# Kernel tuning notes

Measured on AMD Instinct MI355X. Metric: run time of the kernel, lower is better.

The kernel has to match this reference:

```python
import jax, jax.numpy as jnp
import numpy as np

# dims (match init_kwargs / input_specs)
D = 768      # embed_dim
H = 12       # num query heads
G = 4        # num kv groups
E = 8        # num experts
K = 2        # experts per token
F = 4 * D    # ffn hidden dim
B, S, T = 2, 1024, 1024
DH = D // H  # head dim = 64
EPS = 1e-6


def setup_inputs() -> dict:
    key = jax.random.key(0)
    ks = jax.random.split(key, 16)

    def p(k, shape, scale=0.02):
        return jax.random.normal(k, shape, jnp.float32) * scale

    inp = {}
    inp['x'] = jax.random.normal(ks[0], (B, S, D), jnp.float32)
    inp['encoder_context'] = jax.random.normal(ks[1], (B, T, D), jnp.float32)
    for n in ('ln1', 'ln2', 'ln3'):
        inp[n + '_scale'] = jnp.ones((D,), jnp.float32)
        inp[n + '_bias'] = jnp.zeros((D,), jnp.float32)
    i = 2
    for pre in ('sa', 'ca'):
        inp[pre + '_wq'] = p(ks[i], (D, H * DH)); i += 1
        inp[pre + '_bq'] = jnp.zeros((H * DH,), jnp.float32)
        inp[pre + '_wk'] = p(ks[i], (D, G * DH)); i += 1
        inp[pre + '_bk'] = jnp.zeros((G * DH,), jnp.float32)
        inp[pre + '_wv'] = p(ks[i], (D, G * DH)); i += 1
        inp[pre + '_bv'] = jnp.zeros((G * DH,), jnp.float32)
        inp[pre + '_wo'] = p(ks[i], (H * DH, D)); i += 1
        inp[pre + '_bo'] = jnp.zeros((D,), jnp.float32)
    inp['gate_w'] = p(ks[i], (D, E)); i += 1
    inp['gate_b'] = jnp.zeros((E,), jnp.float32)
    inp['w1'] = p(ks[i], (E, D, F)); i += 1
    inp['b1'] = jnp.zeros((E, F), jnp.float32)
    inp['w2'] = p(ks[i], (E, F, D)); i += 1
    inp['b2'] = jnp.zeros((E, D), jnp.float32)
    return inp


def _ln(x, scale, bias):
    mu = jnp.mean(x, axis=-1, keepdims=True)
    var = jnp.mean(jnp.square(x - mu), axis=-1, keepdims=True)
    return (x - mu) * jax.lax.rsqrt(var + EPS) * scale + bias


def _gqa(q_in, kv_in, wq, bq, wk, bk, wv, bv, wo, bo, causal):
    Bq, Sq, _ = q_in.shape
    Skv = kv_in.shape[1]
    q = (q_in @ wq + bq).reshape(Bq, Sq, H, DH)
    k = (kv_in @ wk + bk).reshape(Bq, Skv, G, DH)
    v = (kv_in @ wv + bv).reshape(Bq, Skv, G, DH)
    rep = H // G
    k = jnp.repeat(k, rep, axis=2)  # [B,Skv,H,DH]
    v = jnp.repeat(v, rep, axis=2)
    scores = jnp.einsum('bqhd,bkhd->bhqk', q, k) / jnp.sqrt(jnp.asarray(DH, q.dtype))
    if causal:
        cmask = jnp.tril(jnp.ones((Sq, Skv), bool))
        scores = jnp.where(cmask[None, None], scores, jnp.finfo(scores.dtype).min)
    attn = jax.nn.softmax(scores, axis=-1)
    out = jnp.einsum('bhqk,bkhd->bqhd', attn, v).reshape(Bq, Sq, H * DH)
    return out @ wo + bo


def _moe(x, gate_w, gate_b, w1, b1, w2, b2):
    logits = x @ gate_w + gate_b                      # [B,S,E]
    probs = jax.nn.softmax(logits, axis=-1)
    top_v, top_i = jax.lax.top_k(probs, K)            # [B,S,K]
    top_v = top_v / jnp.sum(top_v, axis=-1, keepdims=True)
    combine = jnp.sum(jax.nn.one_hot(top_i, E, dtype=x.dtype) * top_v[..., None], axis=-2)  # [B,S,E]
    h = jax.nn.gelu(jnp.einsum('bsd,edf->ebsf', x, w1) + b1[:, None, None, :])
    y = jnp.einsum('ebsf,efd->ebsd', h, w2) + b2[:, None, None, :]
    return jnp.einsum('ebsd,bse->bsd', y, combine)


def reference(x, encoder_context,
              ln1_scale, ln1_bias, ln2_scale, ln2_bias, ln3_scale, ln3_bias,
              sa_wq, sa_bq, sa_wk, sa_bk, sa_wv, sa_bv, sa_wo, sa_bo,
              ca_wq, ca_bq, ca_wk, ca_bk, ca_wv, ca_bv, ca_wo, ca_bo,
              gate_w, gate_b, w1, b1, w2, b2):
    xn = _ln(x, ln1_scale, ln1_bias)
    x = x + _gqa(xn, xn, sa_wq, sa_bq, sa_wk, sa_bk, sa_wv, sa_bv, sa_wo, sa_bo, causal=True)
    xn = _ln(x, ln2_scale, ln2_bias)
    x = x + _gqa(xn, encoder_context, ca_wq, ca_bq, ca_wk, ca_bk, ca_wv, ca_bv, ca_wo, ca_bo, causal=False)
    xn = _ln(x, ln3_scale, ln3_bias)
    x = x + _moe(xn, gate_w, gate_b, w1, b1, w2, b2)
    return x
```

## Files before the change

### kernel.cpp

```cpp
#include <hip/hip_runtime.h>

#define DEV __device__ __forceinline__

typedef __attribute__((ext_vector_type(4))) float f32x4;
typedef __attribute__((ext_vector_type(8))) short short8;
typedef __attribute__((ext_vector_type(4))) unsigned int u32x4;
typedef __attribute__((ext_vector_type(4))) unsigned short us16x4;

#define D_ 768
#define S_ 1024
#define B_ 2
#define H_ 12
#define G_ 4
#define DH_ 64
#define E_ 8
#define F_ 3072
#define NTOK (B_*S_)

#define GLDS16(g, l) __builtin_amdgcn_global_load_lds( \
    (const __attribute__((address_space(1))) void*)(g), \
    (__attribute__((address_space(3))) void*)(l), 16, 0, 0)

DEV unsigned short f2bf(float f){
  unsigned int b = __float_as_uint(f);
  b += 0x7FFFu + ((b >> 16) & 1u);
  return (unsigned short)(b >> 16);
}
DEV float bf2f(unsigned short h){ return __uint_as_float(((unsigned int)h) << 16); }
DEV unsigned int splitbf_pack(float v){
  unsigned short h = f2bf(v);
  unsigned short l = f2bf(v - bf2f(h));
  return (unsigned int)h | ((unsigned int)l << 16);
}

DEV short8 lds_swz(const unsigned short* base, int row, int chunk){
  return *(const short8*)((const char*)base + row*128 + (((chunk ^ (row & 7)) << 4)));
}

DEV void swz_decode(int Fb, int nPanels, int& m, int& panel){
  int xcd = Fb & 7;
  int a = Fb >> 3;
  int mi = a & 3;
  int pid = (a >> 2)*8 + xcd;
  m = (pid / nPanels)*4 + mi;
  panel = pid % nPanels;
}

__global__ __launch_bounds__(256) void tcast_kernel(const float* __restrict__ W,
                                                    unsigned short* __restrict__ Wh,
                                                    unsigned short* __restrict__ Wl,
                                                    int K, int N){
  __shared__ float tile[32][33];
  long long zoff = (long long)blockIdx.z * K * N;
  const float* Wz = W + zoff;
  int n0 = blockIdx.x*32, k0 = blockIdx.y*32;
  int tx = threadIdx.x, ty = threadIdx.y;
  #pragma unroll
  for (int i=0;i<4;i++){
    int r = ty + i*8;
    tile[r][tx] = Wz[(long long)(k0+r)*N + n0 + tx];
  }
  __syncthreads();
  #pragma unroll
  for (int i=0;i<4;i++){
    int r = ty + i*8;
    float v = tile[tx][r];
    unsigned int hl = splitbf_pack(v);
    long long o = zoff + (long long)(n0+r)*K + k0 + tx;
    Wh[o] = (unsigned short)(hl & 0xFFFFu);
    if (Wl) Wl[o] = (unsigned short)(hl >> 16);
  }
}

__global__ void split_rows(const float* __restrict__ in, int ld, int width,
                           unsigned short* __restrict__ hi, unsigned short* __restrict__ lo){
  long long t = blockIdx.x;
  int c = threadIdx.x*4;
  f32x4 v = *(const f32x4*)(in + t*ld + c);
  unsigned int p0 = splitbf_pack(v.x), p1 = splitbf_pack(v.y);
  unsigned int p2 = splitbf_pack(v.z), p3 = splitbf_pack(v.w);
  us16x4 h, l;
  h.x=(unsigned short)p0; l.x=(unsigned short)(p0>>16);
  h.y=(unsigned short)p1; l.y=(unsigned short)(p1>>16);
  h.z=(unsigned short)p2; l.z=(unsigned short)(p2>>16);
  h.w=(unsigned short)p3; l.w=(unsigned short)(p3>>16);
  *(us16x4*)(hi + t*width + c) = h;
  *(us16x4*)(lo + t*width + c) = l;
}

__global__ void concat_bias(const float* __restrict__ b0, int n0,
                            const float* __restrict__ b1, int n1,
                            const float* __restrict__ b2, int n2,
                            float* __restrict__ out){
  int i = blockIdx.x*256 + threadIdx.x;
  if (i < n0) out[i] = b0[i];
  else if (i < n0+n1) out[i] = b1[i-n0];
  else if (i < n0+n1+n2) out[i] = b2[i-n0-n1];
}

__global__ __launch_bounds__(256) void ln_kernel(const float* __restrict__ x,
                                                 const float* __restrict__ sc,
                                                 const float* __restrict__ bi,
                                                 unsigned short* __restrict__ outh,
                                                 unsigned short* __restrict__ outl,
                                                 float* __restrict__ outf){
  __shared__ float red[8];
  long long row = blockIdx.x;
  const float* xr = x + row*D_;
  int tid = threadIdx.x;
  float v0 = xr[tid], v1 = xr[tid+256], v2 = xr[tid+512];
  float s = v0+v1+v2;
  float q = v0*v0 + v1*v1 + v2*v2;
  #pragma unroll
  for (int off=32; off; off>>=1){ s += __shfl_xor(s, off); q += __shfl_xor(q, off); }
  int lane = tid & 63, w = tid >> 6;
  if (lane == 0){ red[w] = s; red[4+w] = q; }
  __syncthreads();
  s = red[0]+red[1]+red[2]+red[3];
  q = red[4]+red[5]+red[6]+red[7];
  float mu  = s * (1.0f/D_);
  float var = q * (1.0f/D_) - mu*mu;
  float rstd = rsqrtf(var + 1e-6f);
  #pragma unroll
  for (int i=0;i<3;i++){
    int idx = tid + 256*i;
    float vv = (i==0) ? v0 : (i==1) ? v1 : v2;
    float o = (vv - mu)*rstd*sc[idx] + bi[idx];
    unsigned int pk = splitbf_pack(o);
    outh[row*D_ + idx] = (unsigned short)(pk & 0xFFFFu);
    if (outl) outl[row*D_ + idx] = (unsigned short)(pk >> 16);
    if (outf) outf[row*D_ + idx] = o;
  }
}

__global__ __launch_bounds__(256) void gemm3(
    int nX,
    const unsigned short* __restrict__ Ah, const unsigned short* __restrict__ Al, int lda,
    const unsigned short* __restrict__ Wh, const unsigned short* __restrict__ Wl, int K,
    const float* __restrict__ bias,
    const float* __restrict__ resid, int ldr,
    float* __restrict__ Cf, int ldc)
{
  __shared__ __align__(16) unsigned short AshH[128*64];
  __shared__ __align__(16) unsigned short AshL[128*64];
  __shared__ __align__(16) unsigned short BshH[64*64];
  __shared__ __align__(16) unsigned short BshL[64*64];
  int mB, panel;
  swz_decode(blockIdx.x, nX, mB, panel);
  const int r0 = mB*128;
  const int n0 = panel*64;
  const int tid = threadIdx.x;
  const int lane = tid & 63;
  const int wv = tid >> 6;
  const int wr = (wv>>1)*64, wc = (wv&1)*32;
  const int l15 = lane & 15, l4 = lane >> 4;
  const int sr = lane >> 3;
  const int sc = (lane & 7) ^ sr;

  f32x4 acc[4][2];
  #pragma unroll
  for (int i=0;i<4;i++)
    #pragma unroll
    for (int j=0;j<2;j++) acc[i][j] = (f32x4){0.f,0.f,0.f,0.f};

  for (int k0 = 0; k0 < K; k0 += 64){
    #pragma unroll
    for (int i=0;i<4;i++){
      int seg = wv*4 + i;
      long long src = (long long)(r0 + seg*8 + sr)*lda + k0 + sc*8;
      GLDS16(Ah + src, AshH + seg*8*64);
      GLDS16(Al + src, AshL + seg*8*64);
    }
    #pragma unroll
    for (int i=0;i<2;i++){
      int seg = wv*2 + i;
      long long src = (long long)(n0 + seg*8 + sr)*K + k0 + sc*8;
      GLDS16(Wh + src, BshH + seg*8*64);
      GLDS16(Wl + src, BshL + seg*8*64);
    }
    __syncthreads();
    #pragma unroll
    for (int ks=0; ks<2; ks++){
      int chunk = ks*4 + l4;
      short8 bh[2], bl[2];
      #pragma unroll
      for (int fj=0; fj<2; fj++){
        bh[fj] = lds_swz(BshH, wc + fj*16 + l15, chunk);
        bl[fj] = lds_swz(BshL, wc + fj*16 + l15, chunk);
      }
      #pragma unroll
      for (int fi=0; fi<4; fi++){
        short8 ah = lds_swz(AshH, wr + fi*16 + l15, chunk);
        short8 al = lds_swz(AshL, wr + fi*16 + l15, chunk);
        #pragma unroll
        for (int fj=0; fj<2; fj++){
          acc[fi][fj] = __builtin_amdgcn_mfma_f32_16x16x32_bf16(ah, bh[fj], acc[fi][fj], 0,0,0);
          acc[fi][fj] = __builtin_amdgcn_mfma_f32_16x16x32_bf16(al, bh[fj], acc[fi][fj], 0,0,0);
          acc[fi][fj] = __builtin_amdgcn_mfma_f32_16x16x32_bf16(ah, bl[fj], acc[fi][fj], 0,0,0);
        }
      }
    }
    __syncthreads();
  }

  #pragma unroll
  for (int fi=0; fi<4; fi++)
  #pragma unroll
  for (int fj=0; fj<2; fj++)
  #pragma unroll
  for (int reg=0; reg<4; reg++){
    int r = r0 + wr + fi*16 + l4*4 + reg;
    int col = n0 + wc + fj*16 + l15;
    float val = acc[fi][fj][reg] + bias[col];
    if (resid) val += resid[(long long)r*ldr + col];
    Cf[(long long)r*ldc + col] = val;
  }
}

__global__ __launch_bounds__(256) void gemm_nt128(
    int nX, int nzPerE,
    const unsigned short* __restrict__ A, int lda,
    const unsigned short* __restrict__ Wt, long long wstride,
    const float* __restrict__ bias, int bias_stride,
    const int* __restrict__ counts,
    const int* __restrict__ a_idx, int a_idx_stride,
    const int* __restrict__ row_base,
    float* __restrict__ Cf, long long partStride,
    unsigned short* __restrict__ Cb, int ldc,
    int K, int do_gelu)
{
  __shared__ __align__(16) unsigned short As[128*64];
  __shared__ __align__(16) unsigned short Bs[128*64];
  int mB, panel;
  swz_decode(blockIdx.x, nX*E_*nzPerE, mB, panel);
  const int n0 = (panel % nX)*128;
  const int zI = panel / nX;
  const int z = zI / nzPerE;
  const int kp = zI % nzPerE;
  const int Mz = counts[z];
  const int r0 = mB*128;
  if (r0 >= Mz) return;
  const int obase = row_base[z];
  const unsigned short* Wz = Wt + (long long)z*wstride;
  const float* bz = bias + (long long)z*bias_stride;
  const int kLen = K / nzPerE;
  const int kBeg = kp * kLen;
  const int tid = threadIdx.x;
  const int lane = tid & 63;
  const int wv = tid >> 6;
  const int wr = (wv>>1)*64, wc = (wv&1)*64;
  const int l15 = lane & 15, l4 = lane >> 4;
  const int sr = lane >> 3;
  const int sc = (lane & 7) ^ sr;

  long long arow[4];
  #pragma unroll
  for (int i=0;i<4;i++){
    int seg = wv*4 + i;
    int r = r0 + seg*8 + sr;
    int rcl = (r < Mz) ? r : (Mz-1);
    arow[i] = a_idx ? (long long)a_idx[(long long)z*a_idx_stride + rcl]
                    : (long long)(obase + rcl);
  }

  f32x4 acc[4][4];
  #pragma unroll
  for (int i=0;i<4;i++)
    #pragma unroll
    for (int j=0;j<4;j++) acc[i][j] = (f32x4){0.f,0.f,0.f,0.f};

  for (int k0 = kBeg; k0 < kBeg + kLen; k0 += 64){
    #pragma unroll
    for (int i=0;i<4;i++){
      int seg = wv*4 + i;
      GLDS16(A + arow[i]*lda + k0 + sc*8, As + seg*8*64);
      GLDS16(Wz + (long long)(n0 + seg*8 + sr)*K + k0 + sc*8, Bs + seg*8*64);
    }
    __syncthreads();
    #pragma unroll
    for (int ks=0; ks<2; ks++){
      int chunk = ks*4 + l4;
      short8 a[4], b[4];
      #pragma unroll
      for (int f=0; f<4; f++){
        a[f] = lds_swz(As, wr + f*16 + l15, chunk);
        b[f] = lds_swz(Bs, wc + f*16 + l15, chunk);
      }
      #pragma unroll
      for (int fi=0; fi<4; fi++)
        #pragma unroll
        for (int fj=0; fj<4; fj++)
          acc[fi][fj] = __builtin_amdgcn_mfma_f32_16x16x32_bf16(a[fi], b[fj], acc[fi][fj], 0,0,0);
    }
    __syncthreads();
  }

  #pragma unroll
  for (int fi=0; fi<4; fi++)
  #pragma unroll
  for (int fj=0; fj<4; fj++)
  #pragma unroll
  for (int reg=0; reg<4; reg++){
    int r = r0 + wr + fi*16 + l4*4 + reg;
    if (r >= Mz) continue;
    int col = n0 + wc + fj*16 + l15;
    float val = acc[fi][fj][reg] + (kp == 0 ? bz[col] : 0.0f);
    if (do_gelu){
      float xx = val;
      float u = 0.7978845608028654f*(xx + 0.044715f*xx*xx*xx);
      float t = 1.0f - 2.0f/(__expf(2.0f*u) + 1.0f);
      val = 0.5f*xx*(1.0f + t);
    }
    long long orow = (long long)obase + r;
    if (Cf) Cf[kp*partStride + orow*ldc + col] = val;
    if (Cb) Cb[orow*ldc + col] = f2bf(val);
  }
}

__global__ __launch_bounds__(256) void vt_split_kernel(const float* __restrict__ vin,
                                                       int ld, int cofs,
                                                       unsigned short* __restrict__ vth,
                                                       unsigned short* __restrict__ vtl){
  __shared__ float tile[32][33];
  int s0 = blockIdx.x*32, d0 = blockIdx.y*32;
  int bg = blockIdx.z; int b = bg >> 2, g = bg & 3;
  int tx = threadIdx.x, ty = threadIdx.y;
  #pragma unroll
  for (int i=0;i<4;i++){
    int r = ty + i*8;
    tile[r][tx] = vin[(long long)(b*1024 + s0 + r)*ld + cofs + g*64 + d0 + tx];
  }
  __syncthreads();
  #pragma unroll
  for (int i=0;i<4;i++){
    int d = d0 + ty + i*8;
    unsigned int pk = splitbf_pack(tile[tx][ty + i*8]);
    long long o = (long long)(bg*64 + d)*1024 + s0 + tx;
    vth[o] = (unsigned short)(pk & 0xFFFFu);
    vtl[o] = (unsigned short)(pk >> 16);
  }
}

#define AT_LDK 72
#define AT_LDP 76
__global__ __launch_bounds__(256, 2) void attn_mfma(
    const float* __restrict__ q, int qld,
    const unsigned short* __restrict__ kh, const unsigned short* __restrict__ kl,
    const unsigned short* __restrict__ vth, const unsigned short* __restrict__ vtl,
    unsigned short* __restrict__ ctxh, unsigned short* __restrict__ ctxl, int causal)
{
  __shared__ __align__(16) unsigned short KhS[64*AT_LDK];
  __shared__ __align__(16) unsigned short KlS[64*AT_LDK];
  __shared__ __align__(16) unsigned short VhS[64*AT_LDK];
  __shared__ __align__(16) unsigned short VlS[64*AT_LDK];
  __shared__ __align__(16) unsigned int   Pp[4][16*AT_LDP];

  const int qblk = blockIdx.x;
  const int h = blockIdx.y;
  const int b = blockIdx.z;
  const int g = h / (H_/G_);
  const int tid = threadIdx.x;
  const int lane = tid & 63;
  const int w = tid >> 6;
  const int l15 = lane & 15;
  const int l4 = lane >> 4;
  const int qb0 = qblk*64;

  short8 qh[2], ql[2];
  #pragma unroll
  for (int ks=0; ks<2; ks++){
    const float* qp = q + ((long long)(b*S_ + qb0 + w*16 + l15))*qld + h*DH_ + ks*32 + l4*8;
    f32x4 q0 = *(const f32x4*)qp;
    f32x4 q1 = *(const f32x4*)(qp + 4);
    float qq[8] = {q0.x,q0.y,q0.z,q0.w,q1.x,q1.y,q1.z,q1.w};
    #pragma unroll
    for (int j=0;j<8;j++){
      unsigned int pk = splitbf_pack(qq[j]*0.125f);
      qh[ks][j] = (short)(pk & 0xFFFFu);
      ql[ks][j] = (short)(pk >> 16);
    }
  }

  f32x4 o[4];
  #pragma unroll
  for (int fd=0; fd<4; fd++) o[fd] = (f32x4){0.f,0.f,0.f,0.f};
  float m[4]    = {-3.0e38f,-3.0e38f,-3.0e38f,-3.0e38f};
  float lsum[4] = {0.f,0.f,0.f,0.f};

  const int ntiles = causal ? (qblk + 1) : (S_/64);
  for (int kt=0; kt<ntiles; kt++){
    __syncthreads();
    {
      int r = tid >> 2, c = tid & 3;
      long long krow = (long long)(b*S_ + kt*64 + r)*(G_*DH_) + g*DH_;
      long long vrow = (long long)((b*G_ + g)*64 + r)*S_ + kt*64;
      *(u32x4*)&KhS[r*AT_LDK + c*8]     = *(const u32x4*)(kh + krow + c*8);
      *(u32x4*)&KhS[r*AT_LDK + (c+4)*8] = *(const u32x4*)(kh + krow + (c+4)*8);
      *(u32x4*)&KlS[r*AT_LDK + c*8]     = *(const u32x4*)(kl + krow + c*8);
      *(u32x4*)&KlS[r*AT_LDK + (c+4)*8] = *(const u32x4*)(kl + krow + (c+4)*8);
      *(u32x4*)&VhS[r*AT_LDK + c*8]     = *(const u32x4*)(vth + vrow + c*8);
      *(u32x4*)&VhS[r*AT_LDK + (c+4)*8] = *(const u32x4*)(vth + vrow + (c+4)*8);
      *(u32x4*)&VlS[r*AT_LDK + c*8]     = *(const u32x4*)(vtl + vrow + c*8);
      *(u32x4*)&VlS[r*AT_LDK + (c+4)*8] = *(const u32x4*)(vtl + vrow + (c+4)*8);
    }
    __syncthreads();

    f32x4 s[4];
    #pragma unroll
    for (int fj=0; fj<4; fj++) s[fj] = (f32x4){0.f,0.f,0.f,0.f};
    #pragma unroll
    for (int ks=0; ks<2; ks++){
      #pragma unroll
      for (int fj=0; fj<4; fj++){
        short8 bh = *(const short8*)&KhS[(fj*16 + l15)*AT_LDK + ks*32 + l4*8];
        short8 bl = *(const short8*)&KlS[(fj*16 + l15)*AT_LDK + ks*32 + l4*8];
        s[fj] = __builtin_amdgcn_mfma_f32_16x16x32_bf16(qh[ks], bh, s[fj], 0,0,0);
        s[fj] = __builtin_amdgcn_mfma_f32_16x16x32_bf16(ql[ks], bh, s[fj], 0,0,0);
        s[fj] = __builtin_amdgcn_mfma_f32_16x16x32_bf16(qh[ks], bl, s[fj], 0,0,0);
      }
    }

    if (causal && kt == qblk){
      #pragma unroll
      for (int fj=0; fj<4; fj++){
        int key = kt*64 + fj*16 + l15;
        #pragma unroll
        for (int reg=0; reg<4; reg++){
          int qr = qb0 + w*16 + l4*4 + reg;
          if (key > qr) s[fj][reg] = -3.0e38f;
        }
      }
    }

    float c[4], pmax[4];
    #pragma unroll
    for (int reg=0; reg<4; reg++){
      float mx = fmaxf(fmaxf(s[0][reg], s[1][reg]), fmaxf(s[2][reg], s[3][reg]));
      mx = fmaxf(mx, __shfl_xor(mx, 1));
      mx = fmaxf(mx, __shfl_xor(mx, 2));
      mx = fmaxf(mx, __shfl_xor(mx, 4));
      mx = fmaxf(mx, __shfl_xor(mx, 8));
      float mn = fmaxf(m[reg], mx);
      c[reg] = __expf(m[reg] - mn);
      m[reg] = mn;
      pmax[reg] = mn;
    }
    float psum[4] = {0.f,0.f,0.f,0.f};
    #pragma unroll
    for (int fj=0; fj<4; fj++){
      #pragma unroll
      for (int reg=0; reg<4; reg++){
        float pv = __expf(s[fj][reg] - pmax[reg]);
        psum[reg] += pv;
        Pp[w][(l4*4 + reg)*AT_LDP + fj*16 + l15] = splitbf_pack(pv);
      }
    }
    #pragma unroll
    for (int reg=0; reg<4; reg++){
      float ps = psum[reg];
      ps += __shfl_xor(ps, 1); ps += __shfl_xor(ps, 2);
      ps += __shfl_xor(ps, 4); ps += __shfl_xor(ps, 8);
      lsum[reg] = lsum[reg]*c[reg] + ps;
      o[0][reg] *= c[reg]; o[1][reg] *= c[reg];
      o[2][reg] *= c[reg]; o[3][reg] *= c[reg];
    }

    #pragma unroll
    for (int ks=0; ks<2; ks++){
      u32x4 pa = *(const u32x4*)&Pp[w][l15*AT_LDP + ks*32 + l4*8];
      u32x4 pb = *(const u32x4*)&Pp[w][l15*AT_LDP + ks*32 + l4*8 + 4];
      short8 ph, pl;
      #pragma unroll
      for (int j=0;j<4;j++){
        ph[j]   = (short)(pa[j] & 0xFFFFu); pl[j]   = (short)(pa[j] >> 16);
        ph[4+j] = (short)(pb[j] & 0xFFFFu); pl[4+j] = (short)(pb[j] >> 16);
      }
      #pragma unroll
      for (int fd=0; fd<4; fd++){
        short8 vh = *(const short8*)&VhS[(fd*16 + l15)*AT_LDK + ks*32 + l4*8];
        short8 vl = *(const short8*)&VlS[(fd*16 + l15)*AT_LDK + ks*32 + l4*8];
        o[fd] = __builtin_amdgcn_mfma_f32_16x16x32_bf16(ph, vh, o[fd], 0,0,0);
        o[fd] = __builtin_amdgcn_mfma_f32_16x16x32_bf16(pl, vh, o[fd], 0,0,0);
        o[fd] = __builtin_amdgcn_mfma_f32_16x16x32_bf16(ph, vl, o[fd], 0,0,0);
      }
    }
  }

  #pragma unroll
  for (int reg=0; reg<4; reg++){
    float inv = 1.0f / lsum[reg];
    long long tok = b*S_ + qb0 + w*16 + l4*4 + reg;
    #pragma unroll
    for (int fd=0; fd<4; fd++){
      unsigned int pk = splitbf_pack(o[fd][reg]*inv);
      long long oidx = tok*D_ + h*DH_ + fd*16 + l15;
      ctxh[oidx] = (unsigned short)(pk & 0xFFFFu);
      ctxl[oidx] = (unsigned short)(pk >> 16);
    }
  }
}

__global__ __launch_bounds__(256) void gate_kernel(const float* __restrict__ xnf,
                                                   const float* __restrict__ gw,
                                                   const float* __restrict__ gb,
                                                   int* __restrict__ counts,
                                                   int* __restrict__ toklist,
                                                   int* __restrict__ route_e,
                                                   int* __restrict__ route_pos,
                                                   float* __restrict__ route_w){
  int t = blockIdx.x*4 + (threadIdx.x >> 6);
  int lane = threadIdx.x & 63;
  float acc[E_];
  #pragma unroll
  for (int e=0;e<E_;e++) acc[e] = 0.f;
  #pragma unroll
  for (int i=0;i<12;i++){
    int d = lane + 64*i;
    float xv = xnf[(long long)t*D_ + d];
    const float* w = gw + (long long)d*E_;
    #pragma unroll
    for (int e=0;e<E_;e++) acc[e] += xv*w[e];
  }
  #pragma unroll
  for (int off=32; off; off>>=1)
    #pragma unroll
    for (int e=0;e<E_;e++) acc[e] += __shfl_xor(acc[e], off);
  if (lane == 0){
    #pragma unroll
    for (int e=0;e<E_;e++) acc[e] += gb[e];
    int e0 = 0;
    #pragma unroll
    for (int e=1;e<E_;e++) if (acc[e] > acc[e0]) e0 = e;
    int e1 = -1;
    #pragma unroll
    for (int e=0;e<E_;e++) if (e != e0 && (e1 < 0 || acc[e] > acc[e1])) e1 = e;
    float w0 = 1.0f/(1.0f + __expf(acc[e1] - acc[e0]));
    float w1 = 1.0f - w0;
    int p0 = atomicAdd(&counts[e0], 1);
    int p1 = atomicAdd(&counts[e1], 1);
    toklist[e0*NTOK + p0] = t;
    toklist[e1*NTOK + p1] = t;
    route_e[2*t]   = e0; route_e[2*t+1]   = e1;
    route_pos[2*t] = p0; route_pos[2*t+1] = p1;
    route_w[2*t]   = w0; route_w[2*t+1]   = w1;
  }
}

__global__ void offsets_kernel(const int* __restrict__ counts, int* __restrict__ offs){
  if (threadIdx.x == 0){
    int s = 0;
    for (int e=0;e<E_;e++){ offs[e] = s; s += counts[e]; }
  }
}

__global__ __launch_bounds__(192) void combine_kernel(const float* __restrict__ xb,
                                                      const float* __restrict__ y,
                                                      long long partStride,
                                                      const int* __restrict__ route_e,
                                                      const int* __restrict__ route_pos,
                                                      const float* __restrict__ route_w,
                                                      const int* __restrict__ offs,
                                                      float* __restrict__ out){
  int t = blockIdx.x;
  int i = threadIdx.x;
  int e0 = route_e[2*t], e1 = route_e[2*t+1];
  long long s0 = offs[e0] + route_pos[2*t];
  long long s1 = offs[e1] + route_pos[2*t+1];
  float w0 = route_w[2*t], w1 = route_w[2*t+1];
  f32x4 xv = *(const f32x4*)(xb + (long long)t*D_ + i*4);
  f32x4 y0 = (f32x4){0.f,0.f,0.f,0.f};
  f32x4 y1 = (f32x4){0.f,0.f,0.f,0.f};
  #pragma unroll
  for (int kp=0; kp<4; kp++){
    y0 += *(const f32x4*)(y + kp*partStride + s0*D_ + i*4);
    y1 += *(const f32x4*)(y + kp*partStride + s1*D_ + i*4);
  }
  f32x4 o = xv + w0*y0 + w1*y1;
  *(f32x4*)(out + (long long)t*D_ + i*4) = o;
}

extern "C" void kernel_launch(void* const* d_in, const int* in_sizes, int n_in,
                              void* d_out, int out_size, void* d_ws, size_t ws_size,
                              hipStream_t stream) {
  (void)in_sizes; (void)n_in; (void)out_size; (void)ws_size;
  const float* x     = (const float*)d_in[0];
  const float* enc   = (const float*)d_in[1];
  const float* ln1s  = (const float*)d_in[2];
  const float* ln1b  = (const float*)d_in[3];
  const float* ln2s  = (const float*)d_in[4];
  const float* ln2b  = (const float*)d_in[5];
  const float* ln3s  = (const float*)d_in[6];
  const float* ln3b  = (const float*)d_in[7];
  const float* sa_wq = (const float*)d_in[8];
  const float* sa_bq = (const float*)d_in[9];
  const float* sa_wk = (const float*)d_in[10];
  const float* sa_bk = (const float*)d_in[11];
  const float* sa_wv = (const float*)d_in[12];
  const float* sa_bv = (const float*)d_in[13];
  const float* sa_wo = (const float*)d_in[14];
  const float* sa_bo = (const float*)d_in[15];
  const float* ca_wq = (const float*)d_in[16];
  const float* ca_bq = (const float*)d_in[17];
  const float* ca_wk = (const float*)d_in[18];
  const float* ca_bk = (const float*)d_in[19];
  const float* ca_wv = (const float*)d_in[20];
  const float* ca_bv = (const float*)d_in[21];
  const float* ca_wo = (const float*)d_in[22];
  const float* ca_bo = (const float*)d_in[23];
  const float* gate_w= (const float*)d_in[24];
  const float* gate_b= (const float*)d_in[25];
  const float* w1    = (const float*)d_in[26];
  const float* b1    = (const float*)d_in[27];
  const float* w2    = (const float*)d_in[28];
  const float* b2    = (const float*)d_in[29];
  float* out = (float*)d_out;

  char* p = (char*)d_ws;
  auto alloc = [&](size_t bytes)->void*{
    void* r = (void*)p;
    p += (bytes + 255) & ~(size_t)255;
    return r;
  };
  unsigned short* wqkvh_sa = (unsigned short*)alloc((size_t)1280*768*2);
  unsigned short* wqkvl_sa = (unsigned short*)alloc((size_t)1280*768*2);
  unsigned short* woh_sa   = (unsigned short*)alloc((size_t)768*768*2);
  unsigned short* wol_sa   = (unsigned short*)alloc((size_t)768*768*2);
  unsigned short* wqh_ca   = (unsigned short*)alloc((size_t)768*768*2);
  unsigned short* wql_ca   = (unsigned short*)alloc((size_t)768*768*2);
  unsigned short* wkvh_ca  = (unsigned short*)alloc((size_t)512*768*2);
  unsigned short* wkvl_ca  = (unsigned short*)alloc((size_t)512*768*2);
  unsigned short* woh_ca   = (unsigned short*)alloc((size_t)768*768*2);
  unsigned short* wol_ca   = (unsigned short*)alloc((size_t)768*768*2);
  unsigned short* w1T = (unsigned short*)alloc((size_t)E_*D_*F_*2);
  unsigned short* w2T = (unsigned short*)alloc((size_t)E_*D_*F_*2);
  float* bqkv_sa = (float*)alloc(1280*4);
  float* bkv_ca  = (float*)alloc(512*4);
  unsigned short* ench = (unsigned short*)alloc((size_t)NTOK*D_*2);
  unsigned short* encl = (unsigned short*)alloc((size_t)NTOK*D_*2);
  unsigned short* xh   = (unsigned short*)alloc((size_t)NTOK*D_*2);
  unsigned short* xl   = (unsigned short*)alloc((size_t)NTOK*D_*2);
  unsigned short* ctxh = (unsigned short*)alloc((size_t)NTOK*D_*2);
  unsigned short* ctxl = (unsigned short*)alloc((size_t)NTOK*D_*2);
  unsigned short* xn_b = (unsigned short*)alloc((size_t)NTOK*D_*2);
  unsigned short* hbuf = (unsigned short*)alloc((size_t)2*NTOK*F_*2);
  unsigned short* khp   = (unsigned short*)alloc((size_t)NTOK*G_*DH_*2);
  unsigned short* klp   = (unsigned short*)alloc((size_t)NTOK*G_*DH_*2);
  unsigned short* vtp_h = (unsigned short*)alloc((size_t)NTOK*G_*DH_*2);
  unsigned short* vtp_l = (unsigned short*)alloc((size_t)NTOK*G_*DH_*2);
  float* qkvbuf = (float*)alloc((size_t)NTOK*1280*4);
  float* xnf  = (float*)alloc((size_t)NTOK*D_*4);
  float* xbuf = (float*)alloc((size_t)NTOK*D_*4);
  float* ybuf = (float*)alloc((size_t)8*NTOK*D_*4);
  int* counts    = (int*)alloc(E_*4);
  int* offs      = (int*)alloc(E_*4);
  int* toklist   = (int*)alloc((size_t)E_*NTOK*4);
  int* route_e   = (int*)alloc((size_t)2*NTOK*4);
  int* route_pos = (int*)alloc((size_t)2*NTOK*4);
  float* route_w = (float*)alloc((size_t)2*NTOK*4);

  (void)hipMemsetAsync(counts, 0, E_*sizeof(int), stream);

  dim3 tb(32,8);
  tcast_kernel<<<dim3(24,24,1), tb, 0, stream>>>(sa_wq, wqkvh_sa,            wqkvl_sa,            768, 768);
  tcast_kernel<<<dim3( 8,24,1), tb, 0, stream>>>(sa_wk, wqkvh_sa + 768*768,  wqkvl_sa + 768*768,  768, 256);
  tcast_kernel<<<dim3( 8,24,1), tb, 0, stream>>>(sa_wv, wqkvh_sa + 1024*768, wqkvl_sa + 1024*768, 768, 256);
  tcast_kernel<<<dim3(24,24,1), tb, 0, stream>>>(sa_wo, woh_sa, wol_sa, 768, 768);
  tcast_kernel<<<dim3(24,24,1), tb, 0, stream>>>(ca_wq, wqh_ca, wql_ca, 768, 768);
  tcast_kernel<<<dim3( 8,24,1), tb, 0, stream>>>(ca_wk, wkvh_ca,           wkvl_ca,           768, 256);
  tcast_kernel<<<dim3( 8,24,1), tb, 0, stream>>>(ca_wv, wkvh_ca + 256*768, wkvl_ca + 256*768, 768, 256);
  tcast_kernel<<<dim3(24,24,1), tb, 0, stream>>>(ca_wo, woh_ca, wol_ca, 768, 768);
  tcast_kernel<<<dim3(96,24,E_), tb, 0, stream>>>(w1, w1T, nullptr, 768, 3072);
  tcast_kernel<<<dim3(24,96,E_), tb, 0, stream>>>(w2, w2T, nullptr, 3072, 768);
  concat_bias<<<5, 256, 0, stream>>>(sa_bq, 768, sa_bk, 256, sa_bv, 256, bqkv_sa);
  concat_bias<<<2, 256, 0, stream>>>(ca_bk, 256, ca_bv, 256, nullptr, 0, bkv_ca);
  split_rows<<<NTOK, 192, 0, stream>>>(enc, 768, 768, ench, encl);

  ln_kernel<<<NTOK, 256, 0, stream>>>(x, ln1s, ln1b, xh, xl, nullptr);
  gemm3<<<20*16, 256, 0, stream>>>(20, xh, xl, 768, wqkvh_sa, wqkvl_sa, 768,
      bqkv_sa, nullptr, 0, qkvbuf, 1280);
  split_rows<<<NTOK, 64, 0, stream>>>(qkvbuf + 768, 1280, 256, khp, klp);
  vt_split_kernel<<<dim3(32,2,8), tb, 0, stream>>>(qkvbuf, 1280, 1024, vtp_h, vtp_l);
  attn_mfma<<<dim3(16,12,2), 256, 0, stream>>>(qkvbuf, 1280, khp, klp, vtp_h, vtp_l, ctxh, ctxl, 1);
  gemm3<<<12*16, 256, 0, stream>>>(12, ctxh, ctxl, 768, woh_sa, wol_sa, 768,
      sa_bo, x, 768, xbuf, 768);

  ln_kernel<<<NTOK, 256, 0, stream>>>(xbuf, ln2s, ln2b, xh, xl, nullptr);
  gemm3<<<12*16, 256, 0, stream>>>(12, xh, xl, 768, wqh_ca, wql_ca, 768,
      ca_bq, nullptr, 0, qkvbuf, 1280);
  gemm3<<<8*16, 256, 0, stream>>>(8, ench, encl, 768, wkvh_ca, wkvl_ca, 768,
      bkv_ca, nullptr, 0, qkvbuf + 768, 1280);
  split_rows<<<NTOK, 64, 0, stream>>>(qkvbuf + 768, 1280, 256, khp, klp);
  vt_split_kernel<<<dim3(32,2,8), tb, 0, stream>>>(qkvbuf, 1280, 1024, vtp_h, vtp_l);
  attn_mfma<<<dim3(16,12,2), 256, 0, stream>>>(qkvbuf, 1280, khp, klp, vtp_h, vtp_l, ctxh, ctxl, 0);
  gemm3<<<12*16, 256, 0, stream>>>(12, ctxh, ctxl, 768, woh_ca, wol_ca, 768,
      ca_bo, xbuf, 768, xbuf, 768);

  ln_kernel<<<NTOK, 256, 0, stream>>>(xbuf, ln3s, ln3b, xn_b, nullptr, xnf);
  gate_kernel<<<NTOK/4, 256, 0, stream>>>(xnf, gate_w, gate_b,
      counts, toklist, route_e, route_pos, route_w);
  offsets_kernel<<<1, 64, 0, stream>>>(counts, offs);
  gemm_nt128<<<24*16*E_, 256, 0, stream>>>(24, 1, xn_b, 768, w1T, (long long)F_*D_, b1, F_,
      counts, toklist, NTOK, offs, nullptr, 0, hbuf, F_, 768, 1);
  long long partStride = (long long)2*NTOK*D_;
  gemm_nt128<<<6*16*E_*4, 256, 0, stream>>>(6, 4, hbuf, F_, w2T, (long long)F_*D_, b2, D_,
      counts, nullptr, 0, offs, ybuf, partStride, nullptr, 768, F_, 0);
  combine_kernel<<<NTOK, 192, 0, stream>>>(xbuf, ybuf, partStride,
      route_e, route_pos, route_w, offs, out);
}
```

Before: 514.7 us.

## Double-buffer GEMM LDS tiles and use async swizzled LDS loads in attention

The grouped GEMM now keeps two LDS buffers for A and B and issues the global-to-LDS loads for the next K step before computing on the current one, so memory fetch overlaps MFMA work. The attention kernel replaces register-staged K/V tile copies into padded shared memory with direct global_load_lds transfers into an XOR-swizzled layout, read back through lds_swz. This doubles GEMM LDS usage, which may lower occupancy. The GEMM loop has only one barrier per step after the prefetch is issued, so visibility of the next buffer relies on that end-of-iteration sync.

```diff
diff --git a/kernel.cpp b/kernel.cpp
--- a/kernel.cpp
+++ b/kernel.cpp
@@ -229,8 +229,8 @@
     unsigned short* __restrict__ Cb, int ldc,
     int K, int do_gelu)
 {
-  __shared__ __align__(16) unsigned short As[128*64];
-  __shared__ __align__(16) unsigned short Bs[128*64];
+  __shared__ __align__(16) unsigned short As[2][128*64];
+  __shared__ __align__(16) unsigned short Bs[2][128*64];
   int mB, panel;
   swz_decode(blockIdx.x, nX*E_*nzPerE, mB, panel);
   const int n0 = (panel % nX)*128;
@@ -269,22 +269,29 @@
     #pragma unroll
     for (int j=0;j<4;j++) acc[i][j] = (f32x4){0.f,0.f,0.f,0.f};
 
-  for (int k0 = kBeg; k0 < kBeg + kLen; k0 += 64){
+  auto stage = [&](int buf, int k0){
     #pragma unroll
     for (int i=0;i<4;i++){
       int seg = wv*4 + i;
-      GLDS16(A + arow[i]*lda + k0 + sc*8, As + seg*8*64);
-      GLDS16(Wz + (long long)(n0 + seg*8 + sr)*K + k0 + sc*8, Bs + seg*8*64);
-    }
-    __syncthreads();
+      GLDS16(A + arow[i]*lda + k0 + sc*8, &As[buf][seg*8*64]);
+      GLDS16(Wz + (long long)(n0 + seg*8 + sr)*K + k0 + sc*8, &Bs[buf][seg*8*64]);
+    }
+  };
+
+  const int nsteps = kLen >> 6;
+  stage(0, kBeg);
+  __syncthreads();
+  int cur = 0;
+  for (int t=0; t<nsteps; t++){
+    if (t+1 < nsteps) stage(cur^1, kBeg + (t+1)*64);
     #pragma unroll
     for (int ks=0; ks<2; ks++){
       int chunk = ks*4 + l4;
       short8 a[4], b[4];
       #pragma unroll
       for (int f=0; f<4; f++){
-        a[f] = lds_swz(As, wr + f*16 + l15, chunk);
-        b[f] = lds_swz(Bs, wc + f*16 + l15, chunk);
+        a[f] = lds_swz(&As[cur][0], wr + f*16 + l15, chunk);
+        b[f] = lds_swz(&Bs[cur][0], wc + f*16 + l15, chunk);
       }
       #pragma unroll
       for (int fi=0; fi<4; fi++)
@@ -293,6 +300,7 @@
           acc[fi][fj] = __builtin_amdgcn_mfma_f32_16x16x32_bf16(a[fi], b[fj], acc[fi][fj], 0,0,0);
     }
     __syncthreads();
+    cur ^= 1;
   }
 
   #pragma unroll
@@ -341,7 +349,6 @@
   }
 }
 
-#define AT_LDK 72
 #define AT_LDP 76
 __global__ __launch_bounds__(256, 2) void attn_mfma(
     const float* __restrict__ q, int qld,
@@ -349,10 +356,10 @@
     const unsigned short* __restrict__ vth, const unsigned short* __restrict__ vtl,
     unsigned short* __restrict__ ctxh, unsigned short* __restrict__ ctxl, int causal)
 {
-  __shared__ __align__(16) unsigned short KhS[64*AT_LDK];
-  __shared__ __align__(16) unsigned short KlS[64*AT_LDK];
-  __shared__ __align__(16) unsigned short VhS[64*AT_LDK];
-  __shared__ __align__(16) unsigned short VlS[64*AT_LDK];
+  __shared__ __align__(16) unsigned short KhS[64*64];
+  __shared__ __align__(16) unsigned short KlS[64*64];
+  __shared__ __align__(16) unsigned short VhS[64*64];
+  __shared__ __align__(16) unsigned short VlS[64*64];
   __shared__ __align__(16) unsigned int   Pp[4][16*AT_LDP];
 
   const int qblk = blockIdx.x;
@@ -364,6 +371,8 @@
   const int w = tid >> 6;
   const int l15 = lane & 15;
   const int l4 = lane >> 4;
+  const int sr = lane >> 3;
+  const int sc = (lane & 7) ^ sr;
   const int qb0 = qblk*64;
 
   short8 qh[2], ql[2];
@@ -390,18 +399,16 @@
   const int ntiles = causal ? (qblk + 1) : (S_/64);
   for (int kt=0; kt<ntiles; kt++){
     __syncthreads();
-    {
-      int r = tid >> 2, c = tid & 3;
-      long long krow = (long long)(b*S_ + kt*64 + r)*(G_*DH_) + g*DH_;
-      long long vrow = (long long)((b*G_ + g)*64 + r)*S_ + kt*64;
-      *(u32x4*)&KhS[r*AT_LDK + c*8]     = *(const u32x4*)(kh + krow + c*8);
-      *(u32x4*)&KhS[r*AT_LDK + (c+4)*8] = *(const u32x4*)(kh + krow + (c+4)*8);
-      *(u32x4*)&KlS[r*AT_LDK + c*8]     = *(const u32x4*)(kl + krow + c*8);
-      *(u32x4*)&KlS[r*AT_LDK + (c+4)*8] = *(const u32x4*)(kl + krow + (c+4)*8);
-      *(u32x4*)&VhS[r*AT_LDK + c*8]     = *(const u32x4*)(vth + vrow + c*8);
-      *(u32x4*)&VhS[r*AT_LDK + (c+4)*8] = *(const u32x4*)(vth + vrow + (c+4)*8);
-      *(u32x4*)&VlS[r*AT_LDK + c*8]     = *(const u32x4*)(vtl + vrow + c*8);
-      *(u32x4*)&VlS[r*AT_LDK + (c+4)*8] = *(const u32x4*)(vtl + vrow + (c+4)*8);
+    #pragma unroll
+    for (int i=0;i<2;i++){
+      int seg = w*2 + i;
+      int row = seg*8 + sr;
+      long long ksrc = (long long)(b*S_ + kt*64 + row)*(G_*DH_) + g*DH_ + sc*8;
+      long long vsrc = (long long)((b*G_ + g)*64 + row)*S_ + kt*64 + sc*8;
+      GLDS16(kh  + ksrc, KhS + seg*8*64);
+      GLDS16(kl  + ksrc, KlS + seg*8*64);
+      GLDS16(vth + vsrc, VhS + seg*8*64);
+      GLDS16(vtl + vsrc, VlS + seg*8*64);
     }
     __syncthreads();
 
@@ -410,10 +417,11 @@
     for (int fj=0; fj<4; fj++) s[fj] = (f32x4){0.f,0.f,0.f,0.f};
     #pragma unroll
     for (int ks=0; ks<2; ks++){
+      int chunk = ks*4 + l4;
       #pragma unroll
       for (int fj=0; fj<4; fj++){
-        short8 bh = *(const short8*)&KhS[(fj*16 + l15)*AT_LDK + ks*32 + l4*8];
-        short8 bl = *(const short8*)&KlS[(fj*16 + l15)*AT_LDK + ks*32 + l4*8];
+        short8 bh = lds_swz(KhS, fj*16 + l15, chunk);
+        short8 bl = lds_swz(KlS, fj*16 + l15, chunk);
         s[fj] = __builtin_amdgcn_mfma_f32_16x16x32_bf16(qh[ks], bh, s[fj], 0,0,0);
         s[fj] = __builtin_amdgcn_mfma_f32_16x16x32_bf16(ql[ks], bh, s[fj], 0,0,0);
         s[fj] = __builtin_amdgcn_mfma_f32_16x16x32_bf16(qh[ks], bl, s[fj], 0,0,0);
@@ -467,6 +475,7 @@
 
     #pragma unroll
     for (int ks=0; ks<2; ks++){
+      int chunk = ks*4 + l4;
       u32x4 pa = *(const u32x4*)&Pp[w][l15*AT_LDP + ks*32 + l4*8];
       u32x4 pb = *(const u32x4*)&Pp[w][l15*AT_LDP + ks*32 + l4*8 + 4];
       short8 ph, pl;
@@ -477,8 +486,8 @@
       }
       #pragma unroll
       for (int fd=0; fd<4; fd++){
-        short8 vh = *(const short8*)&VhS[(fd*16 + l15)*AT_LDK + ks*32 + l4*8];
-        short8 vl = *(const short8*)&VlS[(fd*16 + l15)*AT_LDK + ks*32 + l4*8];
+        short8 vh = lds_swz(VhS, fd*16 + l15, chunk);
+        short8 vl = lds_swz(VlS, fd*16 + l15, chunk);
         o[fd] = __builtin_amdgcn_mfma_f32_16x16x32_bf16(ph, vh, o[fd], 0,0,0);
         o[fd] = __builtin_amdgcn_mfma_f32_16x16x32_bf16(pl, vh, o[fd], 0,0,0);
         o[fd] = __builtin_amdgcn_mfma_f32_16x16x32_bf16(ph, vl, o[fd], 0,0,0);
```

After: 531.3 us. 3.2% more time.
